# Performance work log

Hardware: AMD Instinct MI355X
Metric: run time of the kernel (lower is better)

Reference implementation:

```python
import jax, jax.numpy as jnp
import numpy as np

N_NODES = 50000
N_EDGES = 600000
N_GRAPHS = 256
IN_C = 128
HID = 128
OUT_C = 2


def setup_inputs() -> dict:
    key = jax.random.key(0)
    ks = jax.random.split(key, 16)
    d = {}
    d["x"] = jax.random.normal(ks[0], (N_NODES, IN_C), jnp.float32)
    d["edge_index"] = jax.random.randint(ks[1], (2, N_EDGES), 0, N_NODES, dtype=jnp.int32)
    d["root_node_idx"] = jax.random.randint(ks[2], (N_GRAPHS,), 0, N_NODES, dtype=jnp.int32)
    d["batch"] = jnp.sort(jax.random.randint(ks[3], (N_NODES,), 0, N_GRAPHS, dtype=jnp.int32))
    dims = [(IN_C, HID), (HID, HID), (HID, HID), (HID, HID)]
    for i, (ci, co) in enumerate(dims, start=1):
        s = 1.0 / np.sqrt(ci)
        d[f"w{i}_l"] = jax.random.uniform(ks[3 + i], (co, ci), jnp.float32, -s, s)
        d[f"b{i}_l"] = jnp.zeros((co,), jnp.float32)
        d[f"w{i}_r"] = jax.random.uniform(ks[7 + i], (co, ci), jnp.float32, -s, s)
    s = 1.0 / np.sqrt(2 * HID)
    d["w_cls"] = jax.random.uniform(ks[12], (OUT_C, 2 * HID), jnp.float32, -s, s)
    d["b_cls"] = jnp.zeros((OUT_C,), jnp.float32)
    return d


def _sage_conv(x, src, tgt, deg_inv, w_l, b_l, w_r):
    # mean aggregation of source features at target nodes (PyG SAGEConv, aggr='mean')
    agg = jax.ops.segment_sum(x[src], tgt, num_segments=N_NODES) * deg_inv  # [N, C]
    # out = lin_l(agg) + lin_r(x); lin_r has no bias in PyG SAGEConv
    return agg @ w_l.T + b_l + x @ w_r.T


def reference(x, edge_index, root_node_idx, batch,
              w1_l, b1_l, w1_r, w2_l, b2_l, w2_r,
              w3_l, b3_l, w3_r, w4_l, b4_l, w4_r,
              w_cls, b_cls):
    src, tgt = edge_index[0], edge_index[1]
    ones_e = jnp.ones((src.shape[0],), x.dtype)
    deg = jax.ops.segment_sum(ones_e, tgt, num_segments=N_NODES)
    deg_inv = (1.0 / jnp.maximum(deg, 1.0))[:, None]  # [N, 1]

    h = jax.nn.relu(_sage_conv(x, src, tgt, deg_inv, w1_l, b1_l, w1_r))
    h = jax.nn.relu(_sage_conv(h, src, tgt, deg_inv, w2_l, b2_l, w2_r))
    h = jax.nn.relu(_sage_conv(h, src, tgt, deg_inv, w3_l, b3_l, w3_r))
    h = jax.nn.relu(_sage_conv(h, src, tgt, deg_inv, w4_l, b4_l, w4_r))

    root_emb = h[root_node_idx]  # [G, HID]
    g_sum = jax.ops.segment_sum(h, batch, num_segments=N_GRAPHS)
    g_cnt = jax.ops.segment_sum(jnp.ones((h.shape[0],), h.dtype), batch, num_segments=N_GRAPHS)
    graph_emb = g_sum / jnp.maximum(g_cnt, 1.0)[:, None]  # [G, HID]

    combined = jnp.concatenate([root_emb, graph_emb], axis=1)  # [G, 2*HID]
    return combined @ w_cls.T + b_cls  # [G, OUT_C]
```

## Files before the change

kernel.cpp:

```cpp
#include <hip/hip_runtime.h>
#include <hip/hip_bf16.h>

#define N_NODES 50000
#define N_EDGES 600000
#define N_GRAPHS 256
#define C 128
#define NB 196

typedef unsigned short ushort;
typedef unsigned int uint;
typedef __attribute__((ext_vector_type(8))) short bfrag8;
typedef __attribute__((ext_vector_type(4))) float facc4;

__device__ __forceinline__ ushort f2bf(float v) {
    uint u = __float_as_uint(v);
    u += 0x7FFFu + ((u >> 16) & 1u);
    return (ushort)(u >> 16);
}
__device__ __forceinline__ float bf2f(ushort u) {
    return __uint_as_float(((uint)u) << 16);
}
__device__ __forceinline__ void fsplit(float v, ushort& h, ushort& l) {
    h = f2bf(v);
    l = f2bf(v - bf2f(h));
}

__global__ void k_deg(const int* __restrict__ tgt, int* __restrict__ deg) {
    int e = blockIdx.x * blockDim.x + threadIdx.x;
    if (e < N_EDGES) atomicAdd(&deg[tgt[e]], 1);
}

__global__ __launch_bounds__(256) void k_bsum(const int* __restrict__ deg,
                                              int* __restrict__ bsum,
                                              float* __restrict__ dinv) {
    __shared__ int ws[4];
    int idx = blockIdx.x * 256 + threadIdx.x;
    int v = (idx < N_NODES) ? deg[idx] : 0;
    if (idx < N_NODES) dinv[idx] = 1.0f / fmaxf((float)v, 1.0f);
    int s = v;
#pragma unroll
    for (int off = 1; off < 64; off <<= 1) s += __shfl_xor(s, off);
    if ((threadIdx.x & 63) == 0) ws[threadIdx.x >> 6] = s;
    __syncthreads();
    if (threadIdx.x == 0) bsum[blockIdx.x] = ws[0] + ws[1] + ws[2] + ws[3];
}

__global__ __launch_bounds__(256) void k_bscan(const int* __restrict__ bsum,
                                               int* __restrict__ boff,
                                               int* __restrict__ rowptr) {
    __shared__ int ws[4];
    int t = threadIdx.x, lane = t & 63, w = t >> 6;
    int v = (t < NB) ? bsum[t] : 0;
    int incl = v;
#pragma unroll
    for (int off = 1; off < 64; off <<= 1) {
        int u = __shfl_up(incl, off);
        if (lane >= off) incl += u;
    }
    if (lane == 63) ws[w] = incl;
    __syncthreads();
    int wo = 0;
    if (w > 0) wo += ws[0];
    if (w > 1) wo += ws[1];
    if (w > 2) wo += ws[2];
    if (t < NB) boff[t] = wo + incl - v;
    if (t == 0) rowptr[N_NODES] = N_EDGES;
}

__global__ __launch_bounds__(256) void k_rowptr(const int* __restrict__ deg,
                                                const int* __restrict__ boff,
                                                int* __restrict__ rowptr) {
    __shared__ int ws[4];
    int b = blockIdx.x, t = threadIdx.x;
    int idx = b * 256 + t;
    int lane = t & 63, w = t >> 6;
    int v = (idx < N_NODES) ? deg[idx] : 0;
    int incl = v;
#pragma unroll
    for (int off = 1; off < 64; off <<= 1) {
        int u = __shfl_up(incl, off);
        if (lane >= off) incl += u;
    }
    if (lane == 63) ws[w] = incl;
    __syncthreads();
    int wo = 0;
    if (w > 0) wo += ws[0];
    if (w > 1) wo += ws[1];
    if (w > 2) wo += ws[2];
    if (idx < N_NODES) rowptr[idx] = boff[b] + wo + incl - v;
}

__global__ void k_fill(const int* __restrict__ src, const int* __restrict__ tgt,
                       const int* __restrict__ rowptr, int* __restrict__ fill,
                       int* __restrict__ csr_src) {
    int e = blockIdx.x * blockDim.x + threadIdx.x;
    if (e >= N_EDGES) return;
    int d = tgt[e];
    int pos = atomicAdd(&fill[d], 1);
    csr_src[rowptr[d] + pos] = src[e];
}

__global__ __launch_bounds__(256) void k_xsplit(const float* __restrict__ x,
                                                ushort* __restrict__ Ahi,
                                                ushort* __restrict__ Alo) {
    int gid = blockIdx.x * 256 + threadIdx.x;
    if (gid >= N_NODES * 32) return;
    int n = gid >> 5, c4 = (gid & 31) << 2;
    float4 v = *(const float4*)(x + (size_t)n * C + c4);
    ushort4 h, l;
    fsplit(v.x, h.x, l.x); fsplit(v.y, h.y, l.y);
    fsplit(v.z, h.z, l.z); fsplit(v.w, h.w, l.w);
    *(ushort4*)(Ahi + (size_t)n * 256 + 128 + c4) = h;
    *(ushort4*)(Alo + (size_t)n * 256 + 128 + c4) = l;
}

struct WPtrs { const float* wl[4]; const float* wr[4]; };
__global__ __launch_bounds__(256) void k_wsplit(WPtrs wp, ushort* __restrict__ BTh,
                                                ushort* __restrict__ BTl) {
    int gid = blockIdx.x * 256 + threadIdx.x;
    if (gid >= 4 * 128 * 256) return;
    int l = gid >> 15;
    int rem = gid & 32767;
    int n = rem >> 8, k = rem & 255;
    float v = (k < 128) ? wp.wl[l][n * 128 + k] : wp.wr[l][n * 128 + (k - 128)];
    ushort h, lo;
    fsplit(v, h, lo);
    BTh[gid] = h;
    BTl[gid] = lo;
}

__global__ __launch_bounds__(256) void k_gather(const ushort* __restrict__ Ahi_r,
                                                const ushort* __restrict__ Alo_r,
                                                ushort* __restrict__ Ahi_w,
                                                ushort* __restrict__ Alo_w,
                                                const int* __restrict__ csr_src,
                                                const int* __restrict__ rowptr,
                                                const float* __restrict__ dinv) {
    int node = blockIdx.x * 16 + (threadIdx.x >> 4);
    if (node >= N_NODES) return;
    int c8 = (threadIdx.x & 15) << 3;
    int s = rowptr[node], e = rowptr[node + 1];
    float a[8] = {0.f, 0.f, 0.f, 0.f, 0.f, 0.f, 0.f, 0.f};
    int j = s;
    for (; j + 3 < e; j += 4) {
        int s0 = csr_src[j], s1 = csr_src[j + 1];
        int s2 = csr_src[j + 2], s3 = csr_src[j + 3];
        bfrag8 h0 = *(const bfrag8*)(Ahi_r + (size_t)s0 * 256 + 128 + c8);
        bfrag8 l0 = *(const bfrag8*)(Alo_r + (size_t)s0 * 256 + 128 + c8);
        bfrag8 h1 = *(const bfrag8*)(Ahi_r + (size_t)s1 * 256 + 128 + c8);
        bfrag8 l1 = *(const bfrag8*)(Alo_r + (size_t)s1 * 256 + 128 + c8);
        bfrag8 h2 = *(const bfrag8*)(Ahi_r + (size_t)s2 * 256 + 128 + c8);
        bfrag8 l2 = *(const bfrag8*)(Alo_r + (size_t)s2 * 256 + 128 + c8);
        bfrag8 h3 = *(const bfrag8*)(Ahi_r + (size_t)s3 * 256 + 128 + c8);
        bfrag8 l3 = *(const bfrag8*)(Alo_r + (size_t)s3 * 256 + 128 + c8);
#pragma unroll
        for (int c = 0; c < 8; c++)
            a[c] += (bf2f((ushort)h0[c]) + bf2f((ushort)l0[c]))
                  + (bf2f((ushort)h1[c]) + bf2f((ushort)l1[c]))
                  + (bf2f((ushort)h2[c]) + bf2f((ushort)l2[c]))
                  + (bf2f((ushort)h3[c]) + bf2f((ushort)l3[c]));
    }
    for (; j < e; j++) {
        int s0 = csr_src[j];
        bfrag8 h0 = *(const bfrag8*)(Ahi_r + (size_t)s0 * 256 + 128 + c8);
        bfrag8 l0 = *(const bfrag8*)(Alo_r + (size_t)s0 * 256 + 128 + c8);
#pragma unroll
        for (int c = 0; c < 8; c++)
            a[c] += bf2f((ushort)h0[c]) + bf2f((ushort)l0[c]);
    }
    float sc = dinv[node];
    bfrag8 oh, ol;
#pragma unroll
    for (int c = 0; c < 8; c++) {
        float v = a[c] * sc;
        ushort hh, ll;
        fsplit(v, hh, ll);
        oh[c] = (short)hh;
        ol[c] = (short)ll;
    }
    *(bfrag8*)(Ahi_w + (size_t)node * 256 + c8) = oh;
    *(bfrag8*)(Alo_w + (size_t)node * 256 + c8) = ol;
}

__global__ __launch_bounds__(256) void k_gemm(const ushort* __restrict__ Ahi,
                                              const ushort* __restrict__ Alo,
                                              const ushort* __restrict__ BTh,
                                              const ushort* __restrict__ BTl,
                                              const float* __restrict__ bl,
                                              ushort* __restrict__ Hhi,
                                              ushort* __restrict__ Hlo) {
    __shared__ __align__(16) short As[32768];
    const int tid = threadIdx.x;
    const int wave = tid >> 6, lane = tid & 63;
    const int m0 = blockIdx.x * 64;
    const int wn = wave * 32;
    const int l15 = lane & 15, lk = (lane >> 4) * 8;

#pragma unroll
    for (int half = 0; half < 2; half++) {
        bfrag8 r[8];
#pragma unroll
        for (int i = 0; i < 8; i++) {
            int gid = (half * 8 + i) * 256 + tid;
            int p = gid >> 11;
            int rem = gid & 2047;
            int mt = rem >> 9;
            int cc = rem & 511;
            int s = cc >> 6, l = cc & 63;
            int row = m0 + mt * 16 + (l & 15);
            if (row >= N_NODES) row = N_NODES - 1;
            const ushort* base = p ? Alo : Ahi;
            r[i] = *(const bfrag8*)(base + (size_t)row * 256 + s * 32 + (l >> 4) * 8);
        }
#pragma unroll
        for (int i = 0; i < 8; i++) {
            int gid = (half * 8 + i) * 256 + tid;
            *(bfrag8*)&As[gid * 8] = r[i];
        }
    }
    __syncthreads();

    const ushort* pBh[2];
    const ushort* pBl[2];
#pragma unroll
    for (int t = 0; t < 2; t++) {
        int n = wn + t * 16 + l15;
        pBh[t] = BTh + n * 256 + lk;
        pBl[t] = BTl + n * 256 + lk;
    }

    facc4 acc[4][2] = {};
#pragma unroll
    for (int s = 0; s < 8; s++) {
        bfrag8 bh[2], blv[2];
#pragma unroll
        for (int t = 0; t < 2; t++) {
            bh[t]  = *(const bfrag8*)(pBh[t] + s * 32);
            blv[t] = *(const bfrag8*)(pBl[t] + s * 32);
        }
        bfrag8 a0[4], a1[4];
#pragma unroll
        for (int mt = 0; mt < 4; mt++) {
            a0[mt] = *(const bfrag8*)&As[(mt * 512 + s * 64 + lane) * 8];
            a1[mt] = *(const bfrag8*)&As[(2048 + mt * 512 + s * 64 + lane) * 8];
        }
#pragma unroll
        for (int mt = 0; mt < 4; mt++)
#pragma unroll
            for (int nt = 0; nt < 2; nt++) {
                acc[mt][nt] = __builtin_amdgcn_mfma_f32_16x16x32_bf16(a0[mt], bh[nt],  acc[mt][nt], 0, 0, 0);
                acc[mt][nt] = __builtin_amdgcn_mfma_f32_16x16x32_bf16(a0[mt], blv[nt], acc[mt][nt], 0, 0, 0);
                acc[mt][nt] = __builtin_amdgcn_mfma_f32_16x16x32_bf16(a1[mt], bh[nt],  acc[mt][nt], 0, 0, 0);
            }
    }
    __syncthreads();

    float* smf = (float*)As;
    const int r4 = (lane >> 4) * 4;
#pragma unroll
    for (int mt = 0; mt < 4; mt++)
#pragma unroll
        for (int nt = 0; nt < 2; nt++) {
            int cl = wn + nt * 16 + l15;
#pragma unroll
            for (int rr = 0; rr < 4; rr++) {
                int rl = mt * 16 + r4 + rr;
                smf[rl * 132 + cl] = acc[mt][nt][rr];
            }
        }
    __syncthreads();
    const int erow = tid >> 2;
    const int ecs = (tid & 3) * 32;
    int grow = m0 + erow;
    if (grow < N_NODES) {
        float vals[32];
#pragma unroll
        for (int q = 0; q < 8; q++) {
            float4 sv = *(const float4*)&smf[erow * 132 + ecs + q * 4];
            float4 bv = *(const float4*)(bl + ecs + q * 4);
            vals[q * 4 + 0] = fmaxf(sv.x + bv.x, 0.f);
            vals[q * 4 + 1] = fmaxf(sv.y + bv.y, 0.f);
            vals[q * 4 + 2] = fmaxf(sv.z + bv.z, 0.f);
            vals[q * 4 + 3] = fmaxf(sv.w + bv.w, 0.f);
        }
#pragma unroll
        for (int q = 0; q < 4; q++) {
            bfrag8 ho, lo;
#pragma unroll
            for (int c = 0; c < 8; c++) {
                ushort hh, ll;
                fsplit(vals[q * 8 + c], hh, ll);
                ho[c] = (short)hh;
                lo[c] = (short)ll;
            }
            *(bfrag8*)(Hhi + (size_t)grow * 256 + 128 + ecs + q * 8) = ho;
            *(bfrag8*)(Hlo + (size_t)grow * 256 + 128 + ecs + q * 8) = lo;
        }
    }
}

__global__ void k_gstart(const int* __restrict__ batch, int* __restrict__ gstart) {
    int g = blockIdx.x * blockDim.x + threadIdx.x;
    if (g > N_GRAPHS) return;
    int lo = 0, hi = N_NODES;
    while (lo < hi) {
        int mid = (lo + hi) >> 1;
        if (batch[mid] < g) lo = mid + 1;
        else hi = mid;
    }
    gstart[g] = lo;
}

__global__ __launch_bounds__(512) void k_pool(const ushort* __restrict__ Ahi,
                                              const ushort* __restrict__ Alo,
                                              const int* __restrict__ gstart,
                                              float* __restrict__ gmean) {
    __shared__ float part[4][C];
    int g = blockIdx.x;
    int c = threadIdx.x & 127, p = threadIdx.x >> 7;
    int s = gstart[g], e = gstart[g + 1];
    float sum = 0.f;
    for (int n = s + p; n < e; n += 4) {
        size_t o = (size_t)n * 256 + 128 + c;
        sum += bf2f(Ahi[o]) + bf2f(Alo[o]);
    }
    part[p][c] = sum;
    __syncthreads();
    if (p == 0) {
        float tot = part[0][c] + part[1][c] + part[2][c] + part[3][c];
        float cnt = fmaxf((float)(e - s), 1.0f);
        gmean[g * C + c] = tot / cnt;
    }
}

__global__ __launch_bounds__(256) void k_final(const ushort* __restrict__ Ahi,
                                               const ushort* __restrict__ Alo,
                                               const float* __restrict__ gmean,
                                               const int* __restrict__ root,
                                               const float* __restrict__ wcls,
                                               const float* __restrict__ bcls,
                                               float* __restrict__ out) {
    __shared__ float red[8];
    int g = blockIdx.x, t = threadIdx.x;
    float v;
    if (t < 128) {
        size_t o = (size_t)root[g] * 256 + 128 + t;
        v = bf2f(Ahi[o]) + bf2f(Alo[o]);
    } else {
        v = gmean[g * C + (t - 128)];
    }
    float p0 = v * wcls[t];
    float p1 = v * wcls[256 + t];
#pragma unroll
    for (int off = 32; off; off >>= 1) {
        p0 += __shfl_down(p0, off);
        p1 += __shfl_down(p1, off);
    }
    int wid = t >> 6;
    if ((t & 63) == 0) { red[wid] = p0; red[4 + wid] = p1; }
    __syncthreads();
    if (t == 0) {
        out[g * 2 + 0] = red[0] + red[1] + red[2] + red[3] + bcls[0];
        out[g * 2 + 1] = red[4] + red[5] + red[6] + red[7] + bcls[1];
    }
}

extern "C" void kernel_launch(void* const* d_in, const int* in_sizes, int n_in,
                              void* d_out, int out_size, void* d_ws, size_t ws_size,
                              hipStream_t stream) {
    const float* x = (const float*)d_in[0];
    const int* ei = (const int*)d_in[1];
    const int* src = ei;
    const int* tgt = ei + N_EDGES;
    const int* root = (const int*)d_in[2];
    const int* batch = (const int*)d_in[3];
    WPtrs wp;
    wp.wl[0] = (const float*)d_in[4];  wp.wr[0] = (const float*)d_in[6];
    wp.wl[1] = (const float*)d_in[7];  wp.wr[1] = (const float*)d_in[9];
    wp.wl[2] = (const float*)d_in[10]; wp.wr[2] = (const float*)d_in[12];
    wp.wl[3] = (const float*)d_in[13]; wp.wr[3] = (const float*)d_in[15];
    const float* blv[4] = {(const float*)d_in[5], (const float*)d_in[8],
                           (const float*)d_in[11], (const float*)d_in[14]};
    const float* wcls = (const float*)d_in[16];
    const float* bcls = (const float*)d_in[17];
    float* out = (float*)d_out;

    ushort* Ahi = (ushort*)d_ws;
    ushort* Alo = Ahi + (size_t)N_NODES * 256;
    ushort* BTh = Alo + (size_t)N_NODES * 256;
    ushort* BTl = BTh + 4 * 128 * 256;
    int* deg = (int*)(BTl + 4 * 128 * 256);
    float* dinv = (float*)(deg + N_NODES);
    int* rowptr = (int*)(dinv + N_NODES);
    int* fill = rowptr + N_NODES + 1;
    int* csr_src = fill + N_NODES;
    int* bsum = csr_src + N_EDGES;
    int* boff = bsum + 256;
    int* gstart = boff + 256;
    float* gmean = (float*)(gstart + 260);

    hipMemsetAsync(deg, 0, N_NODES * sizeof(int), stream);
    hipMemsetAsync(fill, 0, N_NODES * sizeof(int), stream);
    k_deg<<<(N_EDGES + 255) / 256, 256, 0, stream>>>(tgt, deg);
    k_bsum<<<NB, 256, 0, stream>>>(deg, bsum, dinv);
    k_bscan<<<1, 256, 0, stream>>>(bsum, boff, rowptr);
    k_rowptr<<<NB, 256, 0, stream>>>(deg, boff, rowptr);
    k_fill<<<(N_EDGES + 255) / 256, 256, 0, stream>>>(src, tgt, rowptr, fill, csr_src);
    k_gstart<<<1, 512, 0, stream>>>(batch, gstart);
    k_xsplit<<<(N_NODES * 32 + 255) / 256, 256, 0, stream>>>(x, Ahi, Alo);
    k_wsplit<<<(4 * 128 * 256 + 255) / 256, 256, 0, stream>>>(wp, BTh, BTl);

    for (int l = 0; l < 4; l++) {
        k_gather<<<(N_NODES + 15) / 16, 256, 0, stream>>>(Ahi, Alo, Ahi, Alo,
                                                          csr_src, rowptr, dinv);
        k_gemm<<<(N_NODES + 63) / 64, 256, 0, stream>>>(
            Ahi, Alo, BTh + l * 32768, BTl + l * 32768, blv[l], Ahi, Alo);
    }
    k_pool<<<N_GRAPHS, 512, 0, stream>>>(Ahi, Alo, gstart, gmean);
    k_final<<<N_GRAPHS, 256, 0, stream>>>(Ahi, Alo, gmean, root, wcls, bcls, out);
}
```

Before: 527.3 us.

## Fuse neighbor gather into GEMM kernel with ping-pong feature buffers

Each GEMM block now computes the mean-aggregated neighbor features for its 64 rows directly into shared memory, instead of running a separate gather kernel that writes them to global memory and the GEMM reading them back. Feature storage changes from one interleaved 256-wide buffer to two 128-wide ping-pong buffers, so in-place overwrites are avoided. This removes four kernel launches and the global round-trip of the aggregated features. In exchange, each GEMM block runs an irregular gather with only 256 threads per block and the large LDS footprint, which may limit latency hiding. The two degree/fill memsets are also merged into one.

```diff
diff --git a/kernel.cpp b/kernel.cpp
--- a/kernel.cpp
+++ b/kernel.cpp
@@ -101,8 +101,8 @@
 }
 
 __global__ __launch_bounds__(256) void k_xsplit(const float* __restrict__ x,
-                                                ushort* __restrict__ Ahi,
-                                                ushort* __restrict__ Alo) {
+                                                ushort* __restrict__ Hhi,
+                                                ushort* __restrict__ Hlo) {
     int gid = blockIdx.x * 256 + threadIdx.x;
     if (gid >= N_NODES * 32) return;
     int n = gid >> 5, c4 = (gid & 31) << 2;
@@ -110,8 +110,8 @@
     ushort4 h, l;
     fsplit(v.x, h.x, l.x); fsplit(v.y, h.y, l.y);
     fsplit(v.z, h.z, l.z); fsplit(v.w, h.w, l.w);
-    *(ushort4*)(Ahi + (size_t)n * 256 + 128 + c4) = h;
-    *(ushort4*)(Alo + (size_t)n * 256 + 128 + c4) = l;
+    *(ushort4*)(Hhi + (size_t)n * C + c4) = h;
+    *(ushort4*)(Hlo + (size_t)n * C + c4) = l;
 }
 
 struct WPtrs { const float* wl[4]; const float* wr[4]; };
@@ -129,66 +129,16 @@
     BTl[gid] = lo;
 }
 
-__global__ __launch_bounds__(256) void k_gather(const ushort* __restrict__ Ahi_r,
-                                                const ushort* __restrict__ Alo_r,
-                                                ushort* __restrict__ Ahi_w,
-                                                ushort* __restrict__ Alo_w,
-                                                const int* __restrict__ csr_src,
-                                                const int* __restrict__ rowptr,
-                                                const float* __restrict__ dinv) {
-    int node = blockIdx.x * 16 + (threadIdx.x >> 4);
-    if (node >= N_NODES) return;
-    int c8 = (threadIdx.x & 15) << 3;
-    int s = rowptr[node], e = rowptr[node + 1];
-    float a[8] = {0.f, 0.f, 0.f, 0.f, 0.f, 0.f, 0.f, 0.f};
-    int j = s;
-    for (; j + 3 < e; j += 4) {
-        int s0 = csr_src[j], s1 = csr_src[j + 1];
-        int s2 = csr_src[j + 2], s3 = csr_src[j + 3];
-        bfrag8 h0 = *(const bfrag8*)(Ahi_r + (size_t)s0 * 256 + 128 + c8);
-        bfrag8 l0 = *(const bfrag8*)(Alo_r + (size_t)s0 * 256 + 128 + c8);
-        bfrag8 h1 = *(const bfrag8*)(Ahi_r + (size_t)s1 * 256 + 128 + c8);
-        bfrag8 l1 = *(const bfrag8*)(Alo_r + (size_t)s1 * 256 + 128 + c8);
-        bfrag8 h2 = *(const bfrag8*)(Ahi_r + (size_t)s2 * 256 + 128 + c8);
-        bfrag8 l2 = *(const bfrag8*)(Alo_r + (size_t)s2 * 256 + 128 + c8);
-        bfrag8 h3 = *(const bfrag8*)(Ahi_r + (size_t)s3 * 256 + 128 + c8);
-        bfrag8 l3 = *(const bfrag8*)(Alo_r + (size_t)s3 * 256 + 128 + c8);
-#pragma unroll
-        for (int c = 0; c < 8; c++)
-            a[c] += (bf2f((ushort)h0[c]) + bf2f((ushort)l0[c]))
-                  + (bf2f((ushort)h1[c]) + bf2f((ushort)l1[c]))
-                  + (bf2f((ushort)h2[c]) + bf2f((ushort)l2[c]))
-                  + (bf2f((ushort)h3[c]) + bf2f((ushort)l3[c]));
-    }
-    for (; j < e; j++) {
-        int s0 = csr_src[j];
-        bfrag8 h0 = *(const bfrag8*)(Ahi_r + (size_t)s0 * 256 + 128 + c8);
-        bfrag8 l0 = *(const bfrag8*)(Alo_r + (size_t)s0 * 256 + 128 + c8);
-#pragma unroll
-        for (int c = 0; c < 8; c++)
-            a[c] += bf2f((ushort)h0[c]) + bf2f((ushort)l0[c]);
-    }
-    float sc = dinv[node];
-    bfrag8 oh, ol;
-#pragma unroll
-    for (int c = 0; c < 8; c++) {
-        float v = a[c] * sc;
-        ushort hh, ll;
-        fsplit(v, hh, ll);
-        oh[c] = (short)hh;
-        ol[c] = (short)ll;
-    }
-    *(bfrag8*)(Ahi_w + (size_t)node * 256 + c8) = oh;
-    *(bfrag8*)(Alo_w + (size_t)node * 256 + c8) = ol;
-}
-
-__global__ __launch_bounds__(256) void k_gemm(const ushort* __restrict__ Ahi,
-                                              const ushort* __restrict__ Alo,
-                                              const ushort* __restrict__ BTh,
-                                              const ushort* __restrict__ BTl,
-                                              const float* __restrict__ bl,
-                                              ushort* __restrict__ Hhi,
-                                              ushort* __restrict__ Hlo) {
+__global__ __launch_bounds__(256) void k_fused(const ushort* __restrict__ Hhi_r,
+                                               const ushort* __restrict__ Hlo_r,
+                                               const ushort* __restrict__ BTh,
+                                               const ushort* __restrict__ BTl,
+                                               const float* __restrict__ bl,
+                                               const int* __restrict__ csr_src,
+                                               const int* __restrict__ rowptr,
+                                               const float* __restrict__ dinv,
+                                               ushort* __restrict__ Hhi_w,
+                                               ushort* __restrict__ Hlo_w) {
     __shared__ __align__(16) short As[32768];
     const int tid = threadIdx.x;
     const int wave = tid >> 6, lane = tid & 63;
@@ -196,26 +146,86 @@
     const int wn = wave * 32;
     const int l15 = lane & 15, lk = (lane >> 4) * 8;
 
-#pragma unroll
-    for (int half = 0; half < 2; half++) {
+    {
+        const int c8 = (tid & 15) << 3;
+        const int s_idx = c8 >> 5;
+        const int lhi = ((c8 & 31) >> 3) << 4;
+#pragma unroll
+        for (int it = 0; it < 4; it++) {
+            int r = it * 16 + (tid >> 4);
+            int node = m0 + r;
+            float a[8] = {0.f, 0.f, 0.f, 0.f, 0.f, 0.f, 0.f, 0.f};
+            float sc = 0.f;
+            if (node < N_NODES) {
+                int s = rowptr[node], e = rowptr[node + 1];
+                int j = s;
+                for (; j + 3 < e; j += 4) {
+                    int s0 = csr_src[j], s1 = csr_src[j + 1];
+                    int s2 = csr_src[j + 2], s3 = csr_src[j + 3];
+                    bfrag8 h0 = *(const bfrag8*)(Hhi_r + (size_t)s0 * C + c8);
+                    bfrag8 l0 = *(const bfrag8*)(Hlo_r + (size_t)s0 * C + c8);
+                    bfrag8 h1 = *(const bfrag8*)(Hhi_r + (size_t)s1 * C + c8);
+                    bfrag8 l1 = *(const bfrag8*)(Hlo_r + (size_t)s1 * C + c8);
+                    bfrag8 h2 = *(const bfrag8*)(Hhi_r + (size_t)s2 * C + c8);
+                    bfrag8 l2 = *(const bfrag8*)(Hlo_r + (size_t)s2 * C + c8);
+                    bfrag8 h3 = *(const bfrag8*)(Hhi_r + (size_t)s3 * C + c8);
+                    bfrag8 l3 = *(const bfrag8*)(Hlo_r + (size_t)s3 * C + c8);
+#pragma unroll
+                    for (int c = 0; c < 8; c++)
+                        a[c] += (bf2f((ushort)h0[c]) + bf2f((ushort)l0[c]))
+                              + (bf2f((ushort)h1[c]) + bf2f((ushort)l1[c]))
+                              + (bf2f((ushort)h2[c]) + bf2f((ushort)l2[c]))
+                              + (bf2f((ushort)h3[c]) + bf2f((ushort)l3[c]));
+                }
+                for (; j < e; j++) {
+                    int s0 = csr_src[j];
+                    bfrag8 h0 = *(const bfrag8*)(Hhi_r + (size_t)s0 * C + c8);
+                    bfrag8 l0 = *(const bfrag8*)(Hlo_r + (size_t)s0 * C + c8);
+#pragma unroll
+                    for (int c = 0; c < 8; c++)
+                        a[c] += bf2f((ushort)h0[c]) + bf2f((ushort)l0[c]);
+                }
+                sc = dinv[node];
+            }
+            bfrag8 oh, ol;
+#pragma unroll
+            for (int c = 0; c < 8; c++) {
+                ushort hh, ll;
+                fsplit(a[c] * sc, hh, ll);
+                oh[c] = (short)hh;
+                ol[c] = (short)ll;
+            }
+            int mt = r >> 4;
+            int l = lhi + (r & 15);
+            *(bfrag8*)&As[(mt * 512 + s_idx * 64 + l) * 8] = oh;
+            *(bfrag8*)&As[((4 + mt) * 512 + s_idx * 64 + l) * 8] = ol;
+        }
+    }
+
+    {
         bfrag8 r[8];
 #pragma unroll
         for (int i = 0; i < 8; i++) {
-            int gid = (half * 8 + i) * 256 + tid;
-            int p = gid >> 11;
-            int rem = gid & 2047;
-            int mt = rem >> 9;
-            int cc = rem & 511;
-            int s = cc >> 6, l = cc & 63;
+            int gid = i * 256 + tid;
+            int p = gid >> 10;
+            int rem = gid & 1023;
+            int mt = rem >> 8;
+            int rem2 = rem & 255;
+            int s4 = rem2 >> 6, l = rem2 & 63;
             int row = m0 + mt * 16 + (l & 15);
             if (row >= N_NODES) row = N_NODES - 1;
-            const ushort* base = p ? Alo : Ahi;
-            r[i] = *(const bfrag8*)(base + (size_t)row * 256 + s * 32 + (l >> 4) * 8);
+            const ushort* base = p ? Hlo_r : Hhi_r;
+            r[i] = *(const bfrag8*)(base + (size_t)row * C + s4 * 32 + (l >> 4) * 8);
         }
 #pragma unroll
         for (int i = 0; i < 8; i++) {
-            int gid = (half * 8 + i) * 256 + tid;
-            *(bfrag8*)&As[gid * 8] = r[i];
+            int gid = i * 256 + tid;
+            int p = gid >> 10;
+            int rem = gid & 1023;
+            int mt = rem >> 8;
+            int rem2 = rem & 255;
+            int s4 = rem2 >> 6, l = rem2 & 63;
+            *(bfrag8*)&As[((p * 4 + mt) * 512 + (4 + s4) * 64 + l) * 8] = r[i];
         }
     }
     __syncthreads();
@@ -228,7 +238,6 @@
         pBh[t] = BTh + n * 256 + lk;
         pBl[t] = BTl + n * 256 + lk;
     }
-
     facc4 acc[4][2] = {};
 #pragma unroll
     for (int s = 0; s < 8; s++) {
@@ -293,8 +302,8 @@
                 ho[c] = (short)hh;
                 lo[c] = (short)ll;
             }
-            *(bfrag8*)(Hhi + (size_t)grow * 256 + 128 + ecs + q * 8) = ho;
-            *(bfrag8*)(Hlo + (size_t)grow * 256 + 128 + ecs + q * 8) = lo;
+            *(bfrag8*)(Hhi_w + (size_t)grow * C + ecs + q * 8) = ho;
+            *(bfrag8*)(Hlo_w + (size_t)grow * C + ecs + q * 8) = lo;
         }
     }
 }
@@ -311,8 +320,8 @@
     gstart[g] = lo;
 }
 
-__global__ __launch_bounds__(512) void k_pool(const ushort* __restrict__ Ahi,
-                                              const ushort* __restrict__ Alo,
+__global__ __launch_bounds__(512) void k_pool(const ushort* __restrict__ Hhi,
+                                              const ushort* __restrict__ Hlo,
                                               const int* __restrict__ gstart,
                                               float* __restrict__ gmean) {
     __shared__ float part[4][C];
@@ -321,8 +330,8 @@
     int s = gstart[g], e = gstart[g + 1];
     float sum = 0.f;
     for (int n = s + p; n < e; n += 4) {
-        size_t o = (size_t)n * 256 + 128 + c;
-        sum += bf2f(Ahi[o]) + bf2f(Alo[o]);
+        size_t o = (size_t)n * C + c;
+        sum += bf2f(Hhi[o]) + bf2f(Hlo[o]);
     }
     part[p][c] = sum;
     __syncthreads();
@@ -333,8 +342,8 @@
     }
 }
 
-__global__ __launch_bounds__(256) void k_final(const ushort* __restrict__ Ahi,
-                                               const ushort* __restrict__ Alo,
+__global__ __launch_bounds__(256) void k_final(const ushort* __restrict__ Hhi,
+                                               const ushort* __restrict__ Hlo,
                                                const float* __restrict__ gmean,
                                                const int* __restrict__ root,
                                                const float* __restrict__ wcls,
@@ -344,8 +353,8 @@
     int g = blockIdx.x, t = threadIdx.x;
     float v;
     if (t < 128) {
-        size_t o = (size_t)root[g] * 256 + 128 + t;
-        v = bf2f(Ahi[o]) + bf2f(Alo[o]);
+        size_t o = (size_t)root[g] * C + t;
+        v = bf2f(Hhi[o]) + bf2f(Hlo[o]);
     } else {
         v = gmean[g * C + (t - 128)];
     }
@@ -385,37 +394,40 @@
     const float* bcls = (const float*)d_in[17];
     float* out = (float*)d_out;
 
-    ushort* Ahi = (ushort*)d_ws;
-    ushort* Alo = Ahi + (size_t)N_NODES * 256;
-    ushort* BTh = Alo + (size_t)N_NODES * 256;
+    ushort* H0h = (ushort*)d_ws;
+    ushort* H0l = H0h + (size_t)N_NODES * C;
+    ushort* H1h = H0l + (size_t)N_NODES * C;
+    ushort* H1l = H1h + (size_t)N_NODES * C;
+    ushort* BTh = H1l + (size_t)N_NODES * C;
     ushort* BTl = BTh + 4 * 128 * 256;
     int* deg = (int*)(BTl + 4 * 128 * 256);
-    float* dinv = (float*)(deg + N_NODES);
+    int* fill = deg + N_NODES;
+    float* dinv = (float*)(fill + N_NODES);
     int* rowptr = (int*)(dinv + N_NODES);
-    int* fill = rowptr + N_NODES + 1;
-    int* csr_src = fill + N_NODES;
+    int* csr_src = rowptr + N_NODES + 1;
     int* bsum = csr_src + N_EDGES;
     int* boff = bsum + 256;
     int* gstart = boff + 256;
     float* gmean = (float*)(gstart + 260);
 
-    hipMemsetAsync(deg, 0, N_NODES * sizeof(int), stream);
-    hipMemsetAsync(fill, 0, N_NODES * sizeof(int), stream);
+    hipMemsetAsync(deg, 0, 2 * N_NODES * sizeof(int), stream);
     k_deg<<<(N_EDGES + 255) / 256, 256, 0, stream>>>(tgt, deg);
     k_bsum<<<NB, 256, 0, stream>>>(deg, bsum, dinv);
     k_bscan<<<1, 256, 0, stream>>>(bsum, boff, rowptr);
     k_rowptr<<<NB, 256, 0, stream>>>(deg, boff, rowptr);
     k_fill<<<(N_EDGES + 255) / 256, 256, 0, stream>>>(src, tgt, rowptr, fill, csr_src);
     k_gstart<<<1, 512, 0, stream>>>(batch, gstart);
-    k_xsplit<<<(N_NODES * 32 + 255) / 256, 256, 0, stream>>>(x, Ahi, Alo);
+    k_xsplit<<<(N_NODES * 32 + 255) / 256, 256, 0, stream>>>(x, H0h, H0l);
     k_wsplit<<<(4 * 128 * 256 + 255) / 256, 256, 0, stream>>>(wp, BTh, BTl);
 
+    ushort* Hh[2] = {H0h, H1h};
+    ushort* Hl[2] = {H0l, H1l};
     for (int l = 0; l < 4; l++) {
-        k_gather<<<(N_NODES + 15) / 16, 256, 0, stream>>>(Ahi, Alo, Ahi, Alo,
-                                                          csr_src, rowptr, dinv);
-        k_gemm<<<(N_NODES + 63) / 64, 256, 0, stream>>>(
-            Ahi, Alo, BTh + l * 32768, BTl + l * 32768, blv[l], Ahi, Alo);
-    }
-    k_pool<<<N_GRAPHS, 512, 0, stream>>>(Ahi, Alo, gstart, gmean);
-    k_final<<<N_GRAPHS, 256, 0, stream>>>(Ahi, Alo, gmean, root, wcls, bcls, out);
-}
+        int rb = l & 1, wb = rb ^ 1;
+        k_fused<<<(N_NODES + 63) / 64, 256, 0, stream>>>(
+            Hh[rb], Hl[rb], BTh + l * 32768, BTl + l * 32768, blv[l],
+            csr_src, rowptr, dinv, Hh[wb], Hl[wb]);
+    }
+    k_pool<<<N_GRAPHS, 512, 0, stream>>>(H0h, H0l, gstart, gmean);
+    k_final<<<N_GRAPHS, 256, 0, stream>>>(H0h, H0l, gmean, root, wcls, bcls, out);
+}
```

New measurement: 526.5 us. No clear change (-0.2%).

## Halve GEMM row tile and load A tiles directly into LDS

Applied to the files above, without the earlier changes.

The GEMM kernel now processes 32 rows per block instead of 64, halving LDS use and accumulators and doubling the number of blocks. A tiles are moved with global_load_lds direct-to-LDS transfers instead of going through registers. The two memsets for deg and fill become one by placing the arrays next to each other. This aims to raise occupancy and cut register pressure, at the cost of reloading the B weights in twice as many blocks.

```diff
diff --git a/kernel.cpp b/kernel.cpp
--- a/kernel.cpp
+++ b/kernel.cpp
@@ -189,34 +189,25 @@
                                               const float* __restrict__ bl,
                                               ushort* __restrict__ Hhi,
                                               ushort* __restrict__ Hlo) {
-    __shared__ __align__(16) short As[32768];
+    __shared__ __align__(16) short As[16384];
     const int tid = threadIdx.x;
     const int wave = tid >> 6, lane = tid & 63;
-    const int m0 = blockIdx.x * 64;
+    const int m0 = blockIdx.x * 32;
     const int wn = wave * 32;
     const int l15 = lane & 15, lk = (lane >> 4) * 8;
 
 #pragma unroll
-    for (int half = 0; half < 2; half++) {
-        bfrag8 r[8];
-#pragma unroll
-        for (int i = 0; i < 8; i++) {
-            int gid = (half * 8 + i) * 256 + tid;
-            int p = gid >> 11;
-            int rem = gid & 2047;
-            int mt = rem >> 9;
-            int cc = rem & 511;
-            int s = cc >> 6, l = cc & 63;
-            int row = m0 + mt * 16 + (l & 15);
-            if (row >= N_NODES) row = N_NODES - 1;
-            const ushort* base = p ? Alo : Ahi;
-            r[i] = *(const bfrag8*)(base + (size_t)row * 256 + s * 32 + (l >> 4) * 8);
-        }
-#pragma unroll
-        for (int i = 0; i < 8; i++) {
-            int gid = (half * 8 + i) * 256 + tid;
-            *(bfrag8*)&As[gid * 8] = r[i];
-        }
+    for (int i = 0; i < 8; i++) {
+        int cb = (wave * 8 + i) * 64;
+        int id = cb + lane;
+        int p = id >> 10, mt = (id >> 9) & 1, s = (id >> 6) & 7, l = id & 63;
+        int row = m0 + mt * 16 + (l & 15);
+        if (row >= N_NODES) row = N_NODES - 1;
+        const ushort* gp = (p ? Alo : Ahi) + (size_t)row * 256 + s * 32 + (l >> 4) * 8;
+        __builtin_amdgcn_global_load_lds(
+            (const __attribute__((address_space(1))) uint*)gp,
+            (__attribute__((address_space(3))) uint*)&As[cb * 8],
+            16, 0, 0);
     }
     __syncthreads();
 
@@ -229,7 +220,7 @@
         pBl[t] = BTl + n * 256 + lk;
     }
 
-    facc4 acc[4][2] = {};
+    facc4 acc[2][2] = {};
 #pragma unroll
     for (int s = 0; s < 8; s++) {
         bfrag8 bh[2], blv[2];
@@ -238,14 +229,14 @@
             bh[t]  = *(const bfrag8*)(pBh[t] + s * 32);
             blv[t] = *(const bfrag8*)(pBl[t] + s * 32);
         }
-        bfrag8 a0[4], a1[4];
-#pragma unroll
-        for (int mt = 0; mt < 4; mt++) {
-            a0[mt] = *(const bfrag8*)&As[(mt * 512 + s * 64 + lane) * 8];
-            a1[mt] = *(const bfrag8*)&As[(2048 + mt * 512 + s * 64 + lane) * 8];
+        bfrag8 a0[2], a1[2];
+#pragma unroll
+        for (int mt = 0; mt < 2; mt++) {
+            a0[mt] = *(const bfrag8*)&As[((mt * 8 + s) * 64 + lane) * 8];
+            a1[mt] = *(const bfrag8*)&As[((16 + mt * 8 + s) * 64 + lane) * 8];
         }
 #pragma unroll
-        for (int mt = 0; mt < 4; mt++)
+        for (int mt = 0; mt < 2; mt++)
 #pragma unroll
             for (int nt = 0; nt < 2; nt++) {
                 acc[mt][nt] = __builtin_amdgcn_mfma_f32_16x16x32_bf16(a0[mt], bh[nt],  acc[mt][nt], 0, 0, 0);
@@ -258,7 +249,7 @@
     float* smf = (float*)As;
     const int r4 = (lane >> 4) * 4;
 #pragma unroll
-    for (int mt = 0; mt < 4; mt++)
+    for (int mt = 0; mt < 2; mt++)
 #pragma unroll
         for (int nt = 0; nt < 2; nt++) {
             int cl = wn + nt * 16 + l15;
@@ -269,13 +260,13 @@
             }
         }
     __syncthreads();
-    const int erow = tid >> 2;
-    const int ecs = (tid & 3) * 32;
+    const int erow = tid >> 3;
+    const int ecs = (tid & 7) * 16;
     int grow = m0 + erow;
     if (grow < N_NODES) {
-        float vals[32];
-#pragma unroll
-        for (int q = 0; q < 8; q++) {
+        float vals[16];
+#pragma unroll
+        for (int q = 0; q < 4; q++) {
             float4 sv = *(const float4*)&smf[erow * 132 + ecs + q * 4];
             float4 bv = *(const float4*)(bl + ecs + q * 4);
             vals[q * 4 + 0] = fmaxf(sv.x + bv.x, 0.f);
@@ -284,7 +275,7 @@
             vals[q * 4 + 3] = fmaxf(sv.w + bv.w, 0.f);
         }
 #pragma unroll
-        for (int q = 0; q < 4; q++) {
+        for (int q = 0; q < 2; q++) {
             bfrag8 ho, lo;
 #pragma unroll
             for (int c = 0; c < 8; c++) {
@@ -390,17 +381,16 @@
     ushort* BTh = Alo + (size_t)N_NODES * 256;
     ushort* BTl = BTh + 4 * 128 * 256;
     int* deg = (int*)(BTl + 4 * 128 * 256);
-    float* dinv = (float*)(deg + N_NODES);
+    int* fill = deg + N_NODES;
+    float* dinv = (float*)(fill + N_NODES);
     int* rowptr = (int*)(dinv + N_NODES);
-    int* fill = rowptr + N_NODES + 1;
-    int* csr_src = fill + N_NODES;
+    int* csr_src = rowptr + N_NODES + 1;
     int* bsum = csr_src + N_EDGES;
     int* boff = bsum + 256;
     int* gstart = boff + 256;
     float* gmean = (float*)(gstart + 260);
 
-    hipMemsetAsync(deg, 0, N_NODES * sizeof(int), stream);
-    hipMemsetAsync(fill, 0, N_NODES * sizeof(int), stream);
+    hipMemsetAsync(deg, 0, 2 * N_NODES * sizeof(int), stream);
     k_deg<<<(N_EDGES + 255) / 256, 256, 0, stream>>>(tgt, deg);
     k_bsum<<<NB, 256, 0, stream>>>(deg, bsum, dinv);
     k_bscan<<<1, 256, 0, stream>>>(bsum, boff, rowptr);
@@ -413,7 +403,7 @@
     for (int l = 0; l < 4; l++) {
         k_gather<<<(N_NODES + 15) / 16, 256, 0, stream>>>(Ahi, Alo, Ahi, Alo,
                                                           csr_src, rowptr, dinv);
-        k_gemm<<<(N_NODES + 63) / 64, 256, 0, stream>>>(
+        k_gemm<<<(N_NODES + 31) / 32, 256, 0, stream>>>(
             Ahi, Alo, BTh + l * 32768, BTl + l * 32768, blv[l], Ahi, Alo);
     }
     k_pool<<<N_GRAPHS, 512, 0, stream>>>(Ahi, Alo, gstart, gmean);
```

Measured after the change: 537.5 us. About the same (+1.9%).
